# Performance work log

Measured on AMD Instinct MI355X. Metric: run time of the kernel, lower is better.

The kernel has to match this reference:

```python
import jax, jax.numpy as jnp
import numpy as np

T, D, E, F = 8192, 1024, 8, 3584


def setup_inputs() -> dict:
    key = jax.random.key(0)
    ks = jax.random.split(key, 5)
    scale_in = 1.0 / np.sqrt(D)
    scale_ff = 1.0 / np.sqrt(F)
    return {
        "x": jax.random.normal(ks[0], (T, D), dtype=jnp.float32),
        "w1": jax.random.normal(ks[1], (E, F, D), dtype=jnp.float32) * scale_in,
        "w3": jax.random.normal(ks[2], (E, F, D), dtype=jnp.float32) * scale_in,
        "w2": jax.random.normal(ks[3], (E, D, F), dtype=jnp.float32) * scale_ff,
        "router_logits": jax.random.normal(ks[4], (T, E), dtype=jnp.float32),
        "top_k": 2,
    }


def reference(x, w1, w3, w2, router_logits, top_k):
    # Routing: softmax over experts, keep top-k, renormalize (Mixtral, normalize=True)
    probs = jax.nn.softmax(router_logits, axis=-1)            # [T, E]
    top_vals, top_idx = jax.lax.top_k(probs, top_k)           # [T, k]
    top_vals = top_vals / jnp.sum(top_vals, axis=-1, keepdims=True)
    tokens = jnp.arange(x.shape[0])[:, None]
    weights = jnp.zeros_like(probs).at[tokens, top_idx].set(top_vals)  # [T, E]

    gate = jnp.einsum('td,efd->tef', x, w1)                   # [T, E, F]
    up = jnp.einsum('td,efd->tef', x, w3)                     # [T, E, F]
    h = jax.nn.silu(gate) * up                                # [T, E, F]
    out = jnp.einsum('te,tef,edf->td', weights, h, w2)        # [T, D]
    return out
```

## Files before the change

kernel.cpp:

```cpp
#include <hip/hip_runtime.h>
#include <cstdint>

#define T_TOK 8192
#define D_DIM 1024
#define E_EXP 8
#define F_DIM 3584
#define NROW  (2 * T_TOK)

typedef __attribute__((ext_vector_type(8))) __bf16 bf16x8;
typedef __attribute__((ext_vector_type(4))) float f32x4;

__device__ __forceinline__ void gload16(const void* g, void* l) {
    __builtin_amdgcn_global_load_lds(
        (const __attribute__((address_space(1))) void*)(g),
        (__attribute__((address_space(3))) void*)(l),
        16, 0, 0);
}

__device__ __forceinline__ int xcd_swz(int bid, int nwg) {
    const int nx = 8;
    const int q = nwg / nx, r = nwg % nx;
    const int xcd = bid % nx, lid = bid / nx;
    return (xcd < r ? xcd * (q + 1) : r * (q + 1) + (xcd - r) * q) + lid;
}

__global__ void cvt_kernel(const float* __restrict__ in, __bf16* __restrict__ out, long n) {
    long i = ((long)blockIdx.x * blockDim.x + threadIdx.x) * 8;
    if (i >= n) return;
    const float4 f0 = *(const float4*)(in + i);
    const float4 f1 = *(const float4*)(in + i + 4);
    bf16x8 o;
    o[0] = (__bf16)f0.x; o[1] = (__bf16)f0.y; o[2] = (__bf16)f0.z; o[3] = (__bf16)f0.w;
    o[4] = (__bf16)f1.x; o[5] = (__bf16)f1.y; o[6] = (__bf16)f1.z; o[7] = (__bf16)f1.w;
    *(bf16x8*)(out + i) = o;
}

__global__ void route_kernel(const float* __restrict__ rl, int* cnt,
                             int* __restrict__ eidx, float* __restrict__ ewgt) {
    int t = blockIdx.x * blockDim.x + threadIdx.x;
    if (t >= T_TOK) return;
    float l[8];
#pragma unroll
    for (int e = 0; e < 8; ++e) l[e] = rl[t * 8 + e];
    int i0 = 0; float v0 = l[0];
    int i1 = -1; float v1 = -1e30f;
#pragma unroll
    for (int e = 1; e < 8; ++e) {
        if (l[e] > v0) { v1 = v0; i1 = i0; v0 = l[e]; i0 = e; }
        else if (l[e] > v1) { v1 = l[e]; i1 = e; }
    }
    float wsec = 1.f / (1.f + __expf(v0 - v1));
    eidx[2 * t] = i0; eidx[2 * t + 1] = i1;
    ewgt[2 * t] = 1.f - wsec; ewgt[2 * t + 1] = wsec;
    atomicAdd(&cnt[i0], 1); atomicAdd(&cnt[i1], 1);
}

__global__ void scan_kernel(const int* __restrict__ cnt, int* __restrict__ offs) {
    if (threadIdx.x == 0) {
        int a = 0;
        for (int e = 0; e < E_EXP; ++e) { offs[e] = a; a += cnt[e]; }
        offs[E_EXP] = a;
    }
}

__global__ void assign_kernel(const int* __restrict__ eidx, const float* __restrict__ ewgt,
                              const int* __restrict__ offs, int* cnt2,
                              int* __restrict__ tok, int* __restrict__ rowOf) {
    int t = blockIdx.x * blockDim.x + threadIdx.x;
    if (t >= T_TOK) return;
#pragma unroll
    for (int s = 0; s < 2; ++s) {
        int e = eidx[2 * t + s];
        int pos = atomicAdd(&cnt2[e], 1);
        int row = offs[e] + pos;
        tok[row] = t;
        rowOf[2 * t + s] = row;
    }
}

__device__ __forceinline__ int chunk_row(int c) { return ((c >> 7) << 4) | ((c >> 2) & 15); }
__device__ __forceinline__ int chunk_col(int c) {
    return ((c >> 6) & 1) * 32 + (((c & 3) * 8) ^ (((c >> 5) & 1) << 4));
}

template <int NT>
__device__ __forceinline__ void moe_pipeline(
    const __bf16* const (&srcA)[2][2], const __bf16* const (&srcB)[2][2],
    __bf16 (&Ash)[2][2][8192], __bf16 (&Bsh)[2][2][8192],
    int wave, int abase, int wm, int bh, int bsel, f32x4 (&acc)[8][4])
{
    auto stA = [&](int buf, int kt, int h) {
        const int k0 = kt * 64;
        gload16(srcA[h][0] + k0, &Ash[buf][h][(0 * 512 + wave * 64) * 8]);
        gload16(srcA[h][1] + k0, &Ash[buf][h][(1 * 512 + wave * 64) * 8]);
    };
    auto stB = [&](int buf, int kt, int h) {
        const int k0 = kt * 64;
        gload16(srcB[h][0] + k0, &Bsh[buf][h][(0 * 512 + wave * 64) * 8]);
        gload16(srcB[h][1] + k0, &Bsh[buf][h][(1 * 512 + wave * 64) * 8]);
    };

    bf16x8 bfr[4][2];
    bf16x8 a0, a1, a2, a3;

#define LD_A(Ab, q) \
    a0 = *(const bf16x8*)((Ab) + ((2*(q)) * 2 + 0) * 512); \
    a1 = *(const bf16x8*)((Ab) + ((2*(q)) * 2 + 1) * 512); \
    a2 = *(const bf16x8*)((Ab) + ((2*(q)+1) * 2 + 0) * 512); \
    a3 = *(const bf16x8*)((Ab) + ((2*(q)+1) * 2 + 1) * 512);

#define LD_B(Bb) \
    _Pragma("unroll") for (int ni = 0; ni < 4; ++ni) { \
        bfr[ni][0] = *(const bf16x8*)((Bb) + ((bsel * 4 + ni) * 2 + 0) * 512); \
        bfr[ni][1] = *(const bf16x8*)((Bb) + ((bsel * 4 + ni) * 2 + 1) * 512); \
    }

#define MFMA_Q(q) \
    _Pragma("unroll") for (int ni = 0; ni < 4; ++ni) { \
        acc[2*(q)][ni]   = __builtin_amdgcn_mfma_f32_16x16x32_bf16(a0, bfr[ni][0], acc[2*(q)][ni], 0, 0, 0); \
        acc[2*(q)][ni]   = __builtin_amdgcn_mfma_f32_16x16x32_bf16(a1, bfr[ni][1], acc[2*(q)][ni], 0, 0, 0); \
        acc[2*(q)+1][ni] = __builtin_amdgcn_mfma_f32_16x16x32_bf16(a2, bfr[ni][0], acc[2*(q)+1][ni], 0, 0, 0); \
        acc[2*(q)+1][ni] = __builtin_amdgcn_mfma_f32_16x16x32_bf16(a3, bfr[ni][1], acc[2*(q)+1][ni], 0, 0, 0); \
    }

#define PH_OPEN() \
    __builtin_amdgcn_sched_barrier(0); \
    __builtin_amdgcn_s_barrier(); \
    asm volatile("s_waitcnt lgkmcnt(0)" ::: "memory"); \
    __builtin_amdgcn_sched_barrier(0); \
    __builtin_amdgcn_s_setprio(1);

#define PH_CLOSE() \
    __builtin_amdgcn_s_setprio(0); \
    __builtin_amdgcn_sched_barrier(0); \
    __builtin_amdgcn_s_barrier(); \
    __builtin_amdgcn_sched_barrier(0);

#define PH_CLOSE_G(lastf) \
    __builtin_amdgcn_s_setprio(0); \
    __builtin_amdgcn_sched_barrier(0); \
    if (lastf) { asm volatile("s_waitcnt vmcnt(0)" ::: "memory"); } \
    else       { asm volatile("s_waitcnt vmcnt(4)" ::: "memory"); } \
    __builtin_amdgcn_s_barrier(); \
    __builtin_amdgcn_sched_barrier(0);

    stA(0, 0, 0); stA(0, 0, 1); stB(0, 0, 0); stB(0, 0, 1);
    stB(1, 1, 0); stB(1, 1, 1);
    asm volatile("s_waitcnt vmcnt(4)" ::: "memory");
    __builtin_amdgcn_s_barrier();

    const __bf16* AbE = &Ash[0][wm][abase];
    const __bf16* BbE = &Bsh[0][bh][abase];
    const __bf16* AbO = &Ash[1][wm][abase];
    const __bf16* BbO = &Bsh[1][bh][abase];

    for (int it = 0; it < NT / 2; ++it) {
        const int kv = 2 * it + 1;
        const bool last = (it == NT / 2 - 1);
        LD_A(AbE, 0) LD_B(BbE)
        stA(1, kv, 0);
        PH_OPEN() MFMA_Q(0) PH_CLOSE()
        LD_A(AbE, 1)
        stA(1, kv, 1);
        PH_OPEN() MFMA_Q(1) PH_CLOSE()
        LD_A(AbE, 2)
        if (!last) stB(0, kv + 1, 0);
        PH_OPEN() MFMA_Q(2) PH_CLOSE()
        LD_A(AbE, 3)
        if (!last) stB(0, kv + 1, 1);
        PH_OPEN() MFMA_Q(3) PH_CLOSE_G(last)
        LD_A(AbO, 0) LD_B(BbO)
        if (!last) stA(0, kv + 1, 0);
        PH_OPEN() MFMA_Q(0) PH_CLOSE()
        LD_A(AbO, 1)
        if (!last) stA(0, kv + 1, 1);
        PH_OPEN() MFMA_Q(1) PH_CLOSE()
        LD_A(AbO, 2)
        if (!last) stB(1, kv + 2, 0);
        PH_OPEN() MFMA_Q(2) PH_CLOSE()
        LD_A(AbO, 3)
        if (!last) stB(1, kv + 2, 1);
        PH_OPEN() MFMA_Q(3) PH_CLOSE_G(last)
    }
#undef LD_A
#undef LD_B
#undef MFMA_Q
#undef PH_OPEN
#undef PH_CLOSE
#undef PH_CLOSE_G
}

__global__ __launch_bounds__(512, 1)
void gemm1_kernel(const __bf16* __restrict__ xb,
                  const __bf16* __restrict__ w1b,
                  const __bf16* __restrict__ w3b,
                  const int* __restrict__ tok_of_row,
                  const int* __restrict__ offs,
                  __bf16* __restrict__ h) {
    const int NX = F_DIM / 128, NY = T_TOK / 256;
    const int nwg = NX * NY * E_EXP;
    int w = xcd_swz(blockIdx.x + NX * (blockIdx.y + NY * blockIdx.z), nwg);
    const int nt = w % NX; w /= NX;
    const int mt = w % NY; w /= NY;
    const int e = w;
    const int row0 = offs[e];
    const int rows = offs[e + 1] - row0;
    if (mt * 256 >= rows) return;

    __shared__ __align__(16) __bf16 Ash[2][2][8192];
    __shared__ __align__(16) __bf16 Bsh[2][2][8192];

    const int tid = threadIdx.x;
    const int wave = tid >> 6, lane = tid & 63;
    const int wm = wave >> 2, wn = wave & 3;
    const int fr = lane & 15, fg = lane >> 4;

    const __bf16* srcA[2][2];
    const __bf16* srcB[2][2];
#pragma unroll
    for (int half = 0; half < 2; ++half)
#pragma unroll
        for (int j = 0; j < 2; ++j) {
            const int c = tid + j * 512;
            const int r = chunk_row(c), k = chunk_col(c);
            int ra = mt * 256 + half * 128 + r;
            ra = min(ra, rows - 1);
            srcA[half][j] = xb + (long)tok_of_row[row0 + ra] * D_DIM + k;
            const int rb = half * 128 + r;
            const int blk = rb >> 4;
            const int f = nt * 128 + (blk >> 1) * 16 + (rb & 15);
            const __bf16* wsel = (blk & 1) ? w3b : w1b;
            srcB[half][j] = wsel + ((long)e * F_DIM + f) * D_DIM + k;
        }

    const int abase = fr * 32 + ((fg * 8) ^ ((fr & 8) << 1));
    f32x4 acc[8][4] = {};

    moe_pipeline<16>(srcA, srcB, Ash, Bsh, wave, abase, wm, wn >> 1, wn & 1, acc);

#pragma unroll
    for (int mi = 0; mi < 8; ++mi) {
#pragma unroll
        for (int reg = 0; reg < 4; ++reg) {
            const int lm = mt * 256 + wm * 128 + mi * 16 + fg * 4 + reg;
            if (lm < rows) {
                const long hrow = (long)(row0 + lm) * F_DIM;
#pragma unroll
                for (int b = 0; b < 2; ++b) {
                    const float g = acc[mi][2 * b][reg];
                    const float u = acc[mi][2 * b + 1][reg];
                    const float s = g / (1.f + __expf(-g));
                    h[hrow + nt * 128 + (wn * 2 + b) * 16 + fr] = (__bf16)(s * u);
                }
            }
        }
    }
}

__global__ __launch_bounds__(512, 1)
void gemm2_kernel(const __bf16* __restrict__ h,
                  const __bf16* __restrict__ w2b,
                  const int* __restrict__ offs,
                  __bf16* __restrict__ o2p) {
    const int NX = D_DIM / 256, NY = T_TOK / 256, NZ = E_EXP * 4;
    const int nwg = NX * NY * NZ;
    int w = xcd_swz(blockIdx.x + NX * (blockIdx.y + NY * blockIdx.z), nwg);
    const int nt = w % NX; w /= NX;
    const int mt = w % NY; w /= NY;
    const int e = w >> 2, ks = w & 3;
    const int row0 = offs[e];
    const int rows = offs[e + 1] - row0;
    if (mt * 256 >= rows) return;

    __shared__ __align__(16) __bf16 Ash[2][2][8192];
    __shared__ __align__(16) __bf16 Bsh[2][2][8192];

    const int tid = threadIdx.x;
    const int wave = tid >> 6, lane = tid & 63;
    const int wm = wave >> 2, wn = wave & 3;
    const int fr = lane & 15, fg = lane >> 4;
    const int kofs = ks * 14 * 64;

    const __bf16* srcA[2][2];
    const __bf16* srcB[2][2];
#pragma unroll
    for (int half = 0; half < 2; ++half)
#pragma unroll
        for (int j = 0; j < 2; ++j) {
            const int c = tid + j * 512;
            const int r = chunk_row(c), k = chunk_col(c) + kofs;
            int ra = mt * 256 + half * 128 + r;
            ra = min(ra, rows - 1);
            srcA[half][j] = h + (long)(row0 + ra) * F_DIM + k;
            const int rb = half * 128 + r;
            srcB[half][j] = w2b + ((long)e * D_DIM + nt * 256 + rb) * F_DIM + k;
        }

    const int abase = fr * 32 + ((fg * 8) ^ ((fr & 8) << 1));
    f32x4 acc[8][4] = {};

    moe_pipeline<14>(srcA, srcB, Ash, Bsh, wave, abase, wm, wn >> 1, wn & 1, acc);

    __bf16* ps = o2p + (long)ks * NROW * D_DIM;
#pragma unroll
    for (int mi = 0; mi < 8; ++mi) {
#pragma unroll
        for (int reg = 0; reg < 4; ++reg) {
            const int lm = mt * 256 + wm * 128 + mi * 16 + fg * 4 + reg;
            if (lm < rows) {
                const long obase = (long)(row0 + lm) * D_DIM + nt * 256 + wn * 64 + fr;
#pragma unroll
                for (int ni = 0; ni < 4; ++ni)
                    ps[obase + ni * 16] = (__bf16)acc[mi][ni][reg];
            }
        }
    }
}

__global__ void combine_kernel(const __bf16* __restrict__ o2p, const int* __restrict__ rowOf,
                               const float* __restrict__ ewgt, float* __restrict__ out) {
    const int idx = blockIdx.x * blockDim.x + threadIdx.x;
    const int t = idx >> 7;
    const int j = (idx & 127) * 8;
    const long r0 = rowOf[2 * t], r1 = rowOf[2 * t + 1];
    const float w0 = ewgt[2 * t], w1 = ewgt[2 * t + 1];
    float r[8] = {0, 0, 0, 0, 0, 0, 0, 0};
#pragma unroll
    for (int s = 0; s < 4; ++s) {
        const bf16x8 a = *(const bf16x8*)(o2p + ((long)s * NROW + r0) * D_DIM + j);
        const bf16x8 b = *(const bf16x8*)(o2p + ((long)s * NROW + r1) * D_DIM + j);
#pragma unroll
        for (int q = 0; q < 8; ++q) r[q] += w0 * (float)a[q] + w1 * (float)b[q];
    }
    float4* ob = (float4*)(out + (long)t * D_DIM + j);
    ob[0] = make_float4(r[0], r[1], r[2], r[3]);
    ob[1] = make_float4(r[4], r[5], r[6], r[7]);
}

extern "C" void kernel_launch(void* const* d_in, const int* in_sizes, int n_in,
                              void* d_out, int out_size, void* d_ws, size_t ws_size,
                              hipStream_t stream) {
    const float* x  = (const float*)d_in[0];
    const float* w1 = (const float*)d_in[1];
    const float* w3 = (const float*)d_in[2];
    const float* w2 = (const float*)d_in[3];
    const float* rl = (const float*)d_in[4];
    float* out = (float*)d_out;

    char* ws = (char*)d_ws;
    size_t off = 0;
    auto alloc = [&](size_t bytes) {
        void* p = ws + off;
        off += (bytes + 255) & ~(size_t)255;
        return p;
    };
    __bf16* xb   = (__bf16*)alloc((size_t)T_TOK * D_DIM * 2);
    __bf16* w1b  = (__bf16*)alloc((size_t)E_EXP * F_DIM * D_DIM * 2);
    __bf16* w3b  = (__bf16*)alloc((size_t)E_EXP * F_DIM * D_DIM * 2);
    __bf16* w2b  = (__bf16*)alloc((size_t)E_EXP * D_DIM * F_DIM * 2);
    __bf16* h    = (__bf16*)alloc((size_t)NROW * F_DIM * 2);
    int*   tok   = (int*)alloc(NROW * 4);
    int*   rowOf = (int*)alloc(NROW * 4);
    int*   eidx  = (int*)alloc(NROW * 4);
    float* ewgt  = (float*)alloc(NROW * 4);
    int*   cnt1  = (int*)alloc(64);
    int*   cnt2  = (int*)alloc(64);
    int*   offs  = (int*)alloc(64);
    __bf16* o2p  = xb;

    hipMemsetAsync(cnt1, 0, 64, stream);
    hipMemsetAsync(cnt2, 0, 64, stream);

    {
        long n = (long)T_TOK * D_DIM;
        cvt_kernel<<<(int)(n / 8 / 256), 256, 0, stream>>>(x, xb, n);
        n = (long)E_EXP * F_DIM * D_DIM;
        const int blks = (int)(n / 8 / 256);
        cvt_kernel<<<blks, 256, 0, stream>>>(w1, w1b, n);
        cvt_kernel<<<blks, 256, 0, stream>>>(w3, w3b, n);
        cvt_kernel<<<blks, 256, 0, stream>>>(w2, w2b, n);
    }

    route_kernel<<<T_TOK / 256, 256, 0, stream>>>(rl, cnt1, eidx, ewgt);
    scan_kernel<<<1, 64, 0, stream>>>(cnt1, offs);
    assign_kernel<<<T_TOK / 256, 256, 0, stream>>>(eidx, ewgt, offs, cnt2, tok, rowOf);

    dim3 g1(F_DIM / 128, T_TOK / 256, E_EXP);
    gemm1_kernel<<<g1, 512, 0, stream>>>(xb, w1b, w3b, tok, offs, h);

    dim3 g2(D_DIM / 256, T_TOK / 256, E_EXP * 4);
    gemm2_kernel<<<g2, 512, 0, stream>>>(h, w2b, offs, o2p);

    combine_kernel<<<T_TOK * (D_DIM / 8) / 256, 256, 0, stream>>>(o2p, rowOf, ewgt, out);
}
```

Baseline: 709.8 us.

## Gather tokens into padded per-expert rows and retile GEMMs with triple buffering

Adds a gather kernel that casts routed token rows to bf16 in a per-expert buffer padded to multiples of 256. GEMM loads then use contiguous rows with no per-row token indirection or row bounds checks. Both grouped GEMMs move to smaller tiles (64-wide F for gemm1, 128-wide D for gemm2) with a three-stage LDS pipeline, and gemm2's split-K drops from 4 to 2, which halves the partial-sum traffic in combine. The w2 conversion moves to after gemm1 so w2b and o2p can reuse the workspace region. In exchange, padded rows add wasted compute and smaller tiles reduce operand reuse.

```diff
diff --git a/kernel.cpp b/kernel.cpp
--- a/kernel.cpp
+++ b/kernel.cpp
@@ -6,6 +6,7 @@
 #define E_EXP 8
 #define F_DIM 3584
 #define NROW  (2 * T_TOK)
+#define PROWS_PAD 18432
 
 typedef __attribute__((ext_vector_type(8))) __bf16 bf16x8;
 typedef __attribute__((ext_vector_type(4))) float f32x4;
@@ -55,73 +56,48 @@
     atomicAdd(&cnt[i0], 1); atomicAdd(&cnt[i1], 1);
 }
 
-__global__ void scan_kernel(const int* __restrict__ cnt, int* __restrict__ offs) {
+__global__ void scan_kernel(const int* __restrict__ cnt, int* __restrict__ pofs) {
     if (threadIdx.x == 0) {
         int a = 0;
-        for (int e = 0; e < E_EXP; ++e) { offs[e] = a; a += cnt[e]; }
-        offs[E_EXP] = a;
-    }
-}
-
-__global__ void assign_kernel(const int* __restrict__ eidx, const float* __restrict__ ewgt,
-                              const int* __restrict__ offs, int* cnt2,
-                              int* __restrict__ tok, int* __restrict__ rowOf) {
+        for (int e = 0; e < E_EXP; ++e) { pofs[e] = a; a += (cnt[e] + 255) & ~255; }
+        pofs[E_EXP] = a;
+    }
+}
+
+__global__ void assign_kernel(const int* __restrict__ eidx, const int* __restrict__ pofs,
+                              int* cnt2, int* __restrict__ tokOf, int* __restrict__ rowOf) {
     int t = blockIdx.x * blockDim.x + threadIdx.x;
     if (t >= T_TOK) return;
 #pragma unroll
     for (int s = 0; s < 2; ++s) {
         int e = eidx[2 * t + s];
         int pos = atomicAdd(&cnt2[e], 1);
-        int row = offs[e] + pos;
-        tok[row] = t;
-        rowOf[2 * t + s] = row;
-    }
+        int prow = pofs[e] + pos;
+        tokOf[prow] = t;
+        rowOf[2 * t + s] = prow;
+    }
+}
+
+__global__ void gather_kernel(const float* __restrict__ x, const int* __restrict__ tokOf,
+                              __bf16* __restrict__ xg) {
+    const int idx = blockIdx.x * blockDim.x + threadIdx.x;
+    const int pr = idx >> 7;
+    const int j = (idx & 127) * 8;
+    const int tk = tokOf[pr];
+    bf16x8 o = {};
+    if (tk >= 0) {
+        const float4 f0 = *(const float4*)(x + (long)tk * D_DIM + j);
+        const float4 f1 = *(const float4*)(x + (long)tk * D_DIM + j + 4);
+        o[0] = (__bf16)f0.x; o[1] = (__bf16)f0.y; o[2] = (__bf16)f0.z; o[3] = (__bf16)f0.w;
+        o[4] = (__bf16)f1.x; o[5] = (__bf16)f1.y; o[6] = (__bf16)f1.z; o[7] = (__bf16)f1.w;
+    }
+    *(bf16x8*)(xg + (long)pr * D_DIM + j) = o;
 }
 
 __device__ __forceinline__ int chunk_row(int c) { return ((c >> 7) << 4) | ((c >> 2) & 15); }
 __device__ __forceinline__ int chunk_col(int c) {
     return ((c >> 6) & 1) * 32 + (((c & 3) * 8) ^ (((c >> 5) & 1) << 4));
 }
-
-template <int NT>
-__device__ __forceinline__ void moe_pipeline(
-    const __bf16* const (&srcA)[2][2], const __bf16* const (&srcB)[2][2],
-    __bf16 (&Ash)[2][2][8192], __bf16 (&Bsh)[2][2][8192],
-    int wave, int abase, int wm, int bh, int bsel, f32x4 (&acc)[8][4])
-{
-    auto stA = [&](int buf, int kt, int h) {
-        const int k0 = kt * 64;
-        gload16(srcA[h][0] + k0, &Ash[buf][h][(0 * 512 + wave * 64) * 8]);
-        gload16(srcA[h][1] + k0, &Ash[buf][h][(1 * 512 + wave * 64) * 8]);
-    };
-    auto stB = [&](int buf, int kt, int h) {
-        const int k0 = kt * 64;
-        gload16(srcB[h][0] + k0, &Bsh[buf][h][(0 * 512 + wave * 64) * 8]);
-        gload16(srcB[h][1] + k0, &Bsh[buf][h][(1 * 512 + wave * 64) * 8]);
-    };
-
-    bf16x8 bfr[4][2];
-    bf16x8 a0, a1, a2, a3;
-
-#define LD_A(Ab, q) \
-    a0 = *(const bf16x8*)((Ab) + ((2*(q)) * 2 + 0) * 512); \
-    a1 = *(const bf16x8*)((Ab) + ((2*(q)) * 2 + 1) * 512); \
-    a2 = *(const bf16x8*)((Ab) + ((2*(q)+1) * 2 + 0) * 512); \
-    a3 = *(const bf16x8*)((Ab) + ((2*(q)+1) * 2 + 1) * 512);
-
-#define LD_B(Bb) \
-    _Pragma("unroll") for (int ni = 0; ni < 4; ++ni) { \
-        bfr[ni][0] = *(const bf16x8*)((Bb) + ((bsel * 4 + ni) * 2 + 0) * 512); \
-        bfr[ni][1] = *(const bf16x8*)((Bb) + ((bsel * 4 + ni) * 2 + 1) * 512); \
-    }
-
-#define MFMA_Q(q) \
-    _Pragma("unroll") for (int ni = 0; ni < 4; ++ni) { \
-        acc[2*(q)][ni]   = __builtin_amdgcn_mfma_f32_16x16x32_bf16(a0, bfr[ni][0], acc[2*(q)][ni], 0, 0, 0); \
-        acc[2*(q)][ni]   = __builtin_amdgcn_mfma_f32_16x16x32_bf16(a1, bfr[ni][1], acc[2*(q)][ni], 0, 0, 0); \
-        acc[2*(q)+1][ni] = __builtin_amdgcn_mfma_f32_16x16x32_bf16(a2, bfr[ni][0], acc[2*(q)+1][ni], 0, 0, 0); \
-        acc[2*(q)+1][ni] = __builtin_amdgcn_mfma_f32_16x16x32_bf16(a3, bfr[ni][1], acc[2*(q)+1][ni], 0, 0, 0); \
-    }
 
 #define PH_OPEN() \
     __builtin_amdgcn_sched_barrier(0); \
@@ -136,183 +112,203 @@
     __builtin_amdgcn_s_barrier(); \
     __builtin_amdgcn_sched_barrier(0);
 
-#define PH_CLOSE_G(lastf) \
+#define PH_CLOSE_GATE() \
     __builtin_amdgcn_s_setprio(0); \
     __builtin_amdgcn_sched_barrier(0); \
-    if (lastf) { asm volatile("s_waitcnt vmcnt(0)" ::: "memory"); } \
-    else       { asm volatile("s_waitcnt vmcnt(4)" ::: "memory"); } \
+    asm volatile("s_waitcnt vmcnt(8)" ::: "memory"); \
     __builtin_amdgcn_s_barrier(); \
     __builtin_amdgcn_sched_barrier(0);
 
-    stA(0, 0, 0); stA(0, 0, 1); stB(0, 0, 0); stB(0, 0, 1);
-    stB(1, 1, 0); stB(1, 1, 1);
-    asm volatile("s_waitcnt vmcnt(4)" ::: "memory");
+template <int NT>
+__device__ __forceinline__ void moe_pipeline(
+    const __bf16* const (&srcA)[2][2], const __bf16* const (&srcB)[2],
+    __bf16 (&Ash)[3][2][8192], __bf16 (&Bsh)[3][8192],
+    int wave, int abase, int ah, int wqm, int wn, f32x4 (&acc)[4][4])
+{
+    auto stA = [&](int buf, int kt, int h) {
+        const long k0 = (long)kt * 64;
+        gload16(srcA[h][0] + k0, &Ash[buf][h][(0 * 512 + wave * 64) * 8]);
+        gload16(srcA[h][1] + k0, &Ash[buf][h][(1 * 512 + wave * 64) * 8]);
+    };
+    auto stB = [&](int buf, int kt) {
+        const long k0 = (long)kt * 64;
+        gload16(srcB[0] + k0, &Bsh[buf][(0 * 512 + wave * 64) * 8]);
+        gload16(srcB[1] + k0, &Bsh[buf][(1 * 512 + wave * 64) * 8]);
+    };
+
+    stA(0, 0, 0); stA(0, 0, 1); stB(0, 0);
+    stB(1, 1); stA(1, 1, 0); stA(1, 1, 1);
+    stB(2, 2);
+    asm volatile("s_waitcnt vmcnt(8)" ::: "memory");
     __builtin_amdgcn_s_barrier();
 
-    const __bf16* AbE = &Ash[0][wm][abase];
-    const __bf16* BbE = &Bsh[0][bh][abase];
-    const __bf16* AbO = &Ash[1][wm][abase];
-    const __bf16* BbO = &Bsh[1][bh][abase];
-
-    for (int it = 0; it < NT / 2; ++it) {
-        const int kv = 2 * it + 1;
-        const bool last = (it == NT / 2 - 1);
-        LD_A(AbE, 0) LD_B(BbE)
-        stA(1, kv, 0);
-        PH_OPEN() MFMA_Q(0) PH_CLOSE()
-        LD_A(AbE, 1)
-        stA(1, kv, 1);
-        PH_OPEN() MFMA_Q(1) PH_CLOSE()
-        LD_A(AbE, 2)
-        if (!last) stB(0, kv + 1, 0);
-        PH_OPEN() MFMA_Q(2) PH_CLOSE()
-        LD_A(AbE, 3)
-        if (!last) stB(0, kv + 1, 1);
-        PH_OPEN() MFMA_Q(3) PH_CLOSE_G(last)
-        LD_A(AbO, 0) LD_B(BbO)
-        if (!last) stA(0, kv + 1, 0);
-        PH_OPEN() MFMA_Q(0) PH_CLOSE()
-        LD_A(AbO, 1)
-        if (!last) stA(0, kv + 1, 1);
-        PH_OPEN() MFMA_Q(1) PH_CLOSE()
-        LD_A(AbO, 2)
-        if (!last) stB(1, kv + 2, 0);
-        PH_OPEN() MFMA_Q(2) PH_CLOSE()
-        LD_A(AbO, 3)
-        if (!last) stB(1, kv + 2, 1);
-        PH_OPEN() MFMA_Q(3) PH_CLOSE_G(last)
-    }
-#undef LD_A
-#undef LD_B
-#undef MFMA_Q
-#undef PH_OPEN
-#undef PH_CLOSE
-#undef PH_CLOSE_G
+    bf16x8 bfr[4][2], afr[2][2];
+
+#pragma unroll
+    for (int t = 0; t < NT; ++t) {
+        const int b0 = t % 3, b2 = (t + 2) % 3;
+        const int k2 = (t + 2 < NT) ? t + 2 : t + 2 - NT;
+        const int k3 = (t + 3 < NT) ? t + 3 : t + 3 - NT;
+        const __bf16* Ab = &Ash[b0][ah][abase];
+        const __bf16* Bb = &Bsh[b0][abase];
+#pragma unroll
+        for (int ni = 0; ni < 4; ++ni)
+#pragma unroll
+            for (int kk = 0; kk < 2; ++kk)
+                bfr[ni][kk] = *(const bf16x8*)(Bb + ((wn * 4 + ni) * 2 + kk) * 512);
+#pragma unroll
+        for (int mi = 0; mi < 2; ++mi)
+#pragma unroll
+            for (int kk = 0; kk < 2; ++kk)
+                afr[mi][kk] = *(const bf16x8*)(Ab + ((wqm * 4 + mi) * 2 + kk) * 512);
+        PH_OPEN()
+        stA(b2, k2, 0); stA(b2, k2, 1);
+#pragma unroll
+        for (int mi = 0; mi < 2; ++mi)
+#pragma unroll
+            for (int ni = 0; ni < 4; ++ni) {
+                acc[mi][ni] = __builtin_amdgcn_mfma_f32_16x16x32_bf16(afr[mi][0], bfr[ni][0], acc[mi][ni], 0, 0, 0);
+                acc[mi][ni] = __builtin_amdgcn_mfma_f32_16x16x32_bf16(afr[mi][1], bfr[ni][1], acc[mi][ni], 0, 0, 0);
+            }
+        PH_CLOSE()
+#pragma unroll
+        for (int mi = 0; mi < 2; ++mi)
+#pragma unroll
+            for (int kk = 0; kk < 2; ++kk)
+                afr[mi][kk] = *(const bf16x8*)(Ab + ((wqm * 4 + 2 + mi) * 2 + kk) * 512);
+        PH_OPEN()
+        stB(b0, k3);
+#pragma unroll
+        for (int mi = 0; mi < 2; ++mi)
+#pragma unroll
+            for (int ni = 0; ni < 4; ++ni) {
+                acc[2 + mi][ni] = __builtin_amdgcn_mfma_f32_16x16x32_bf16(afr[mi][0], bfr[ni][0], acc[2 + mi][ni], 0, 0, 0);
+                acc[2 + mi][ni] = __builtin_amdgcn_mfma_f32_16x16x32_bf16(afr[mi][1], bfr[ni][1], acc[2 + mi][ni], 0, 0, 0);
+            }
+        PH_CLOSE_GATE()
+    }
+    asm volatile("s_waitcnt vmcnt(0)" ::: "memory");
 }
 
 __global__ __launch_bounds__(512, 1)
-void gemm1_kernel(const __bf16* __restrict__ xb,
+void gemm1_kernel(const __bf16* __restrict__ xg,
                   const __bf16* __restrict__ w1b,
                   const __bf16* __restrict__ w3b,
-                  const int* __restrict__ tok_of_row,
-                  const int* __restrict__ offs,
+                  const int* __restrict__ pofs,
                   __bf16* __restrict__ h) {
-    const int NX = F_DIM / 128, NY = T_TOK / 256;
+    const int NX = F_DIM / 64, NY = T_TOK / 256;
     const int nwg = NX * NY * E_EXP;
     int w = xcd_swz(blockIdx.x + NX * (blockIdx.y + NY * blockIdx.z), nwg);
     const int nt = w % NX; w /= NX;
     const int mt = w % NY; w /= NY;
     const int e = w;
-    const int row0 = offs[e];
-    const int rows = offs[e + 1] - row0;
-    if (mt * 256 >= rows) return;
-
-    __shared__ __align__(16) __bf16 Ash[2][2][8192];
-    __shared__ __align__(16) __bf16 Bsh[2][2][8192];
+    const int row0 = pofs[e];
+    const int prows = pofs[e + 1] - row0;
+    if (mt * 256 >= prows) return;
+
+    __shared__ __align__(16) __bf16 Ash[3][2][8192];
+    __shared__ __align__(16) __bf16 Bsh[3][8192];
 
     const int tid = threadIdx.x;
     const int wave = tid >> 6, lane = tid & 63;
-    const int wm = wave >> 2, wn = wave & 3;
+    const int wm = wave >> 1, wn = wave & 1;
     const int fr = lane & 15, fg = lane >> 4;
 
     const __bf16* srcA[2][2];
-    const __bf16* srcB[2][2];
+    const __bf16* srcB[2];
 #pragma unroll
     for (int half = 0; half < 2; ++half)
 #pragma unroll
         for (int j = 0; j < 2; ++j) {
             const int c = tid + j * 512;
-            const int r = chunk_row(c), k = chunk_col(c);
-            int ra = mt * 256 + half * 128 + r;
-            ra = min(ra, rows - 1);
-            srcA[half][j] = xb + (long)tok_of_row[row0 + ra] * D_DIM + k;
-            const int rb = half * 128 + r;
-            const int blk = rb >> 4;
-            const int f = nt * 128 + (blk >> 1) * 16 + (rb & 15);
-            const __bf16* wsel = (blk & 1) ? w3b : w1b;
-            srcB[half][j] = wsel + ((long)e * F_DIM + f) * D_DIM + k;
+            srcA[half][j] = xg + (long)(row0 + mt * 256 + half * 128 + chunk_row(c)) * D_DIM + chunk_col(c);
         }
+#pragma unroll
+    for (int j = 0; j < 2; ++j) {
+        const int c = tid + j * 512;
+        const int rb = chunk_row(c);
+        const int blk = rb >> 4;
+        const int f = nt * 64 + (blk >> 1) * 16 + (rb & 15);
+        srcB[j] = ((blk & 1) ? w3b : w1b) + ((long)e * F_DIM + f) * D_DIM + chunk_col(c);
+    }
 
     const int abase = fr * 32 + ((fg * 8) ^ ((fr & 8) << 1));
-    f32x4 acc[8][4] = {};
-
-    moe_pipeline<16>(srcA, srcB, Ash, Bsh, wave, abase, wm, wn >> 1, wn & 1, acc);
-
-#pragma unroll
-    for (int mi = 0; mi < 8; ++mi) {
+    f32x4 acc[4][4] = {};
+
+    moe_pipeline<D_DIM / 64>(srcA, srcB, Ash, Bsh, wave, abase, wm >> 1, wm & 1, wn, acc);
+
+#pragma unroll
+    for (int mi = 0; mi < 4; ++mi) {
 #pragma unroll
         for (int reg = 0; reg < 4; ++reg) {
-            const int lm = mt * 256 + wm * 128 + mi * 16 + fg * 4 + reg;
-            if (lm < rows) {
-                const long hrow = (long)(row0 + lm) * F_DIM;
-#pragma unroll
-                for (int b = 0; b < 2; ++b) {
-                    const float g = acc[mi][2 * b][reg];
-                    const float u = acc[mi][2 * b + 1][reg];
-                    const float s = g / (1.f + __expf(-g));
-                    h[hrow + nt * 128 + (wn * 2 + b) * 16 + fr] = (__bf16)(s * u);
-                }
+            const int lm = mt * 256 + wm * 64 + mi * 16 + fg * 4 + reg;
+            const long hrow = (long)(row0 + lm) * F_DIM;
+#pragma unroll
+            for (int b = 0; b < 2; ++b) {
+                const float g = acc[mi][2 * b][reg];
+                const float u = acc[mi][2 * b + 1][reg];
+                const float s = g / (1.f + __expf(-g));
+                h[hrow + nt * 64 + (wn * 2 + b) * 16 + fr] = (__bf16)(s * u);
             }
         }
     }
 }
 
 __global__ __launch_bounds__(512, 1)
-void gemm2_kernel(const __bf16* __restrict__ h,
+void gemm2_kernel(const __bf16* __restrict__ hb,
                   const __bf16* __restrict__ w2b,
-                  const int* __restrict__ offs,
+                  const int* __restrict__ pofs,
                   __bf16* __restrict__ o2p) {
-    const int NX = D_DIM / 256, NY = T_TOK / 256, NZ = E_EXP * 4;
-    const int nwg = NX * NY * NZ;
+    const int NX = D_DIM / 128, NY = T_TOK / 256;
+    const int nwg = NX * NY * E_EXP * 2;
     int w = xcd_swz(blockIdx.x + NX * (blockIdx.y + NY * blockIdx.z), nwg);
     const int nt = w % NX; w /= NX;
     const int mt = w % NY; w /= NY;
-    const int e = w >> 2, ks = w & 3;
-    const int row0 = offs[e];
-    const int rows = offs[e + 1] - row0;
-    if (mt * 256 >= rows) return;
-
-    __shared__ __align__(16) __bf16 Ash[2][2][8192];
-    __shared__ __align__(16) __bf16 Bsh[2][2][8192];
+    const int e = w >> 1, ks = w & 1;
+    const int row0 = pofs[e];
+    const int prows = pofs[e + 1] - row0;
+    if (mt * 256 >= prows) return;
+
+    __shared__ __align__(16) __bf16 Ash[3][2][8192];
+    __shared__ __align__(16) __bf16 Bsh[3][8192];
 
     const int tid = threadIdx.x;
     const int wave = tid >> 6, lane = tid & 63;
-    const int wm = wave >> 2, wn = wave & 3;
+    const int wm = wave >> 1, wn = wave & 1;
     const int fr = lane & 15, fg = lane >> 4;
-    const int kofs = ks * 14 * 64;
+    const int kofs = ks * (F_DIM / 2);
 
     const __bf16* srcA[2][2];
-    const __bf16* srcB[2][2];
+    const __bf16* srcB[2];
 #pragma unroll
     for (int half = 0; half < 2; ++half)
 #pragma unroll
         for (int j = 0; j < 2; ++j) {
             const int c = tid + j * 512;
-            const int r = chunk_row(c), k = chunk_col(c) + kofs;
-            int ra = mt * 256 + half * 128 + r;
-            ra = min(ra, rows - 1);
-            srcA[half][j] = h + (long)(row0 + ra) * F_DIM + k;
-            const int rb = half * 128 + r;
-            srcB[half][j] = w2b + ((long)e * D_DIM + nt * 256 + rb) * F_DIM + k;
+            srcA[half][j] = hb + (long)(row0 + mt * 256 + half * 128 + chunk_row(c)) * F_DIM + kofs + chunk_col(c);
         }
+#pragma unroll
+    for (int j = 0; j < 2; ++j) {
+        const int c = tid + j * 512;
+        const int d = nt * 128 + chunk_row(c);
+        srcB[j] = w2b + ((long)e * D_DIM + d) * F_DIM + kofs + chunk_col(c);
+    }
 
     const int abase = fr * 32 + ((fg * 8) ^ ((fr & 8) << 1));
-    f32x4 acc[8][4] = {};
-
-    moe_pipeline<14>(srcA, srcB, Ash, Bsh, wave, abase, wm, wn >> 1, wn & 1, acc);
-
-    __bf16* ps = o2p + (long)ks * NROW * D_DIM;
-#pragma unroll
-    for (int mi = 0; mi < 8; ++mi) {
+    f32x4 acc[4][4] = {};
+
+    moe_pipeline<F_DIM / 2 / 64>(srcA, srcB, Ash, Bsh, wave, abase, wm >> 1, wm & 1, wn, acc);
+
+    __bf16* ps = o2p + (long)ks * PROWS_PAD * D_DIM;
+#pragma unroll
+    for (int mi = 0; mi < 4; ++mi) {
 #pragma unroll
         for (int reg = 0; reg < 4; ++reg) {
-            const int lm = mt * 256 + wm * 128 + mi * 16 + fg * 4 + reg;
-            if (lm < rows) {
-                const long obase = (long)(row0 + lm) * D_DIM + nt * 256 + wn * 64 + fr;
-#pragma unroll
-                for (int ni = 0; ni < 4; ++ni)
-                    ps[obase + ni * 16] = (__bf16)acc[mi][ni][reg];
-            }
+            const int lm = mt * 256 + wm * 64 + mi * 16 + fg * 4 + reg;
+            const long obase = (long)(row0 + lm) * D_DIM + nt * 128 + wn * 64 + fr;
+#pragma unroll
+            for (int ni = 0; ni < 4; ++ni)
+                ps[obase + ni * 16] = (__bf16)acc[mi][ni][reg];
         }
     }
 }
@@ -326,9 +322,9 @@
     const float w0 = ewgt[2 * t], w1 = ewgt[2 * t + 1];
     float r[8] = {0, 0, 0, 0, 0, 0, 0, 0};
 #pragma unroll
-    for (int s = 0; s < 4; ++s) {
-        const bf16x8 a = *(const bf16x8*)(o2p + ((long)s * NROW + r0) * D_DIM + j);
-        const bf16x8 b = *(const bf16x8*)(o2p + ((long)s * NROW + r1) * D_DIM + j);
+    for (int s = 0; s < 2; ++s) {
+        const bf16x8 a = *(const bf16x8*)(o2p + ((long)s * PROWS_PAD + r0) * D_DIM + j);
+        const bf16x8 b = *(const bf16x8*)(o2p + ((long)s * PROWS_PAD + r1) * D_DIM + j);
 #pragma unroll
         for (int q = 0; q < 8; ++q) r[q] += w0 * (float)a[q] + w1 * (float)b[q];
     }
@@ -354,42 +350,46 @@
         off += (bytes + 255) & ~(size_t)255;
         return p;
     };
-    __bf16* xb   = (__bf16*)alloc((size_t)T_TOK * D_DIM * 2);
+    __bf16* xg   = (__bf16*)alloc((size_t)PROWS_PAD * D_DIM * 2);
     __bf16* w1b  = (__bf16*)alloc((size_t)E_EXP * F_DIM * D_DIM * 2);
     __bf16* w3b  = (__bf16*)alloc((size_t)E_EXP * F_DIM * D_DIM * 2);
-    __bf16* w2b  = (__bf16*)alloc((size_t)E_EXP * D_DIM * F_DIM * 2);
-    __bf16* h    = (__bf16*)alloc((size_t)NROW * F_DIM * 2);
-    int*   tok   = (int*)alloc(NROW * 4);
+    __bf16* hbuf = (__bf16*)alloc((size_t)PROWS_PAD * F_DIM * 2);
+    int*   tokOf = (int*)alloc(PROWS_PAD * 4);
     int*   rowOf = (int*)alloc(NROW * 4);
     int*   eidx  = (int*)alloc(NROW * 4);
     float* ewgt  = (float*)alloc(NROW * 4);
     int*   cnt1  = (int*)alloc(64);
     int*   cnt2  = (int*)alloc(64);
-    int*   offs  = (int*)alloc(64);
-    __bf16* o2p  = xb;
+    int*   pofs  = (int*)alloc(64);
+    __bf16* w2b = (__bf16*)ws;
+    __bf16* o2p = (__bf16*)(ws + (size_t)E_EXP * F_DIM * D_DIM * 2);
 
     hipMemsetAsync(cnt1, 0, 64, stream);
     hipMemsetAsync(cnt2, 0, 64, stream);
+    hipMemsetAsync(tokOf, 0xFF, PROWS_PAD * 4, stream);
+
+    route_kernel<<<T_TOK / 256, 256, 0, stream>>>(rl, cnt1, eidx, ewgt);
+    scan_kernel<<<1, 64, 0, stream>>>(cnt1, pofs);
+    assign_kernel<<<T_TOK / 256, 256, 0, stream>>>(eidx, pofs, cnt2, tokOf, rowOf);
+    gather_kernel<<<PROWS_PAD * 128 / 256, 256, 0, stream>>>(x, tokOf, xg);
 
     {
-        long n = (long)T_TOK * D_DIM;
-        cvt_kernel<<<(int)(n / 8 / 256), 256, 0, stream>>>(x, xb, n);
-        n = (long)E_EXP * F_DIM * D_DIM;
+        const long n = (long)E_EXP * F_DIM * D_DIM;
         const int blks = (int)(n / 8 / 256);
         cvt_kernel<<<blks, 256, 0, stream>>>(w1, w1b, n);
         cvt_kernel<<<blks, 256, 0, stream>>>(w3, w3b, n);
-        cvt_kernel<<<blks, 256, 0, stream>>>(w2, w2b, n);
-    }
-
-    route_kernel<<<T_TOK / 256, 256, 0, stream>>>(rl, cnt1, eidx, ewgt);
-    scan_kernel<<<1, 64, 0, stream>>>(cnt1, offs);
-    assign_kernel<<<T_TOK / 256, 256, 0, stream>>>(eidx, ewgt, offs, cnt2, tok, rowOf);
-
-    dim3 g1(F_DIM / 128, T_TOK / 256, E_EXP);
-    gemm1_kernel<<<g1, 512, 0, stream>>>(xb, w1b, w3b, tok, offs, h);
-
-    dim3 g2(D_DIM / 256, T_TOK / 256, E_EXP * 4);
-    gemm2_kernel<<<g2, 512, 0, stream>>>(h, w2b, offs, o2p);
+    }
+
+    dim3 g1(F_DIM / 64, T_TOK / 256, E_EXP);
+    gemm1_kernel<<<g1, 512, 0, stream>>>(xg, w1b, w3b, pofs, hbuf);
+
+    {
+        const long n = (long)E_EXP * D_DIM * F_DIM;
+        cvt_kernel<<<(int)(n / 8 / 256), 256, 0, stream>>>(w2, w2b, n);
+    }
+
+    dim3 g2(D_DIM / 128, T_TOK / 256, E_EXP * 2);
+    gemm2_kernel<<<g2, 512, 0, stream>>>(hbuf, w2b, pofs, o2p);
 
     combine_kernel<<<T_TOK * (D_DIM / 8) / 256, 256, 0, stream>>>(o2p, rowOf, ewgt, out);
 }
```

After: 821.2 us. 1.16x slower.

## Pre-gather padded per-expert activations and halve gemm2 split-K

Applied to the files above, without the earlier changes.

Routing now runs before conversion. Each expert's row block is padded to a multiple of 256, and a gather kernel writes token rows as bf16 into a contiguous, padded activation buffer. This removes the per-row indirect token lookup and the row-bound checks from gemm1's loads and epilogues, and it folds the x conversion into the gather. gemm2's split-K drops from 4 to 2, which halves the partial-output traffic read back by combine but gives each block a longer K loop and fewer blocks. The workspace is rearranged so w2b and the partials alias earlier buffers, which adds a memset and some wasted work on padded rows.

```diff
diff --git a/kernel.cpp b/kernel.cpp
--- a/kernel.cpp
+++ b/kernel.cpp
@@ -6,6 +6,7 @@
 #define E_EXP 8
 #define F_DIM 3584
 #define NROW  (2 * T_TOK)
+#define PROWS_PAD 18432
 
 typedef __attribute__((ext_vector_type(8))) __bf16 bf16x8;
 typedef __attribute__((ext_vector_type(4))) float f32x4;
@@ -55,27 +56,42 @@
     atomicAdd(&cnt[i0], 1); atomicAdd(&cnt[i1], 1);
 }
 
-__global__ void scan_kernel(const int* __restrict__ cnt, int* __restrict__ offs) {
+__global__ void scan_kernel(const int* __restrict__ cnt, int* __restrict__ pofs) {
     if (threadIdx.x == 0) {
         int a = 0;
-        for (int e = 0; e < E_EXP; ++e) { offs[e] = a; a += cnt[e]; }
-        offs[E_EXP] = a;
-    }
-}
-
-__global__ void assign_kernel(const int* __restrict__ eidx, const float* __restrict__ ewgt,
-                              const int* __restrict__ offs, int* cnt2,
-                              int* __restrict__ tok, int* __restrict__ rowOf) {
+        for (int e = 0; e < E_EXP; ++e) { pofs[e] = a; a += (cnt[e] + 255) & ~255; }
+        pofs[E_EXP] = a;
+    }
+}
+
+__global__ void assign_kernel(const int* __restrict__ eidx, const int* __restrict__ pofs,
+                              int* cnt2, int* __restrict__ tokOf, int* __restrict__ rowOf) {
     int t = blockIdx.x * blockDim.x + threadIdx.x;
     if (t >= T_TOK) return;
 #pragma unroll
     for (int s = 0; s < 2; ++s) {
         int e = eidx[2 * t + s];
         int pos = atomicAdd(&cnt2[e], 1);
-        int row = offs[e] + pos;
-        tok[row] = t;
-        rowOf[2 * t + s] = row;
-    }
+        int prow = pofs[e] + pos;
+        tokOf[prow] = t;
+        rowOf[2 * t + s] = prow;
+    }
+}
+
+__global__ void gather_kernel(const float* __restrict__ x, const int* __restrict__ tokOf,
+                              __bf16* __restrict__ xg) {
+    const int idx = blockIdx.x * blockDim.x + threadIdx.x;
+    const int pr = idx >> 7;
+    const int j = (idx & 127) * 8;
+    const int tk = tokOf[pr];
+    bf16x8 o = {};
+    if (tk >= 0) {
+        const float4 f0 = *(const float4*)(x + (long)tk * D_DIM + j);
+        const float4 f1 = *(const float4*)(x + (long)tk * D_DIM + j + 4);
+        o[0] = (__bf16)f0.x; o[1] = (__bf16)f0.y; o[2] = (__bf16)f0.z; o[3] = (__bf16)f0.w;
+        o[4] = (__bf16)f1.x; o[5] = (__bf16)f1.y; o[6] = (__bf16)f1.z; o[7] = (__bf16)f1.w;
+    }
+    *(bf16x8*)(xg + (long)pr * D_DIM + j) = o;
 }
 
 __device__ __forceinline__ int chunk_row(int c) { return ((c >> 7) << 4) | ((c >> 2) & 15); }
@@ -90,12 +106,12 @@
     int wave, int abase, int wm, int bh, int bsel, f32x4 (&acc)[8][4])
 {
     auto stA = [&](int buf, int kt, int h) {
-        const int k0 = kt * 64;
+        const long k0 = (long)kt * 64;
         gload16(srcA[h][0] + k0, &Ash[buf][h][(0 * 512 + wave * 64) * 8]);
         gload16(srcA[h][1] + k0, &Ash[buf][h][(1 * 512 + wave * 64) * 8]);
     };
     auto stB = [&](int buf, int kt, int h) {
-        const int k0 = kt * 64;
+        const long k0 = (long)kt * 64;
         gload16(srcB[h][0] + k0, &Bsh[buf][h][(0 * 512 + wave * 64) * 8]);
         gload16(srcB[h][1] + k0, &Bsh[buf][h][(1 * 512 + wave * 64) * 8]);
     };
@@ -191,11 +207,10 @@
 }
 
 __global__ __launch_bounds__(512, 1)
-void gemm1_kernel(const __bf16* __restrict__ xb,
+void gemm1_kernel(const __bf16* __restrict__ xg,
                   const __bf16* __restrict__ w1b,
                   const __bf16* __restrict__ w3b,
-                  const int* __restrict__ tok_of_row,
-                  const int* __restrict__ offs,
+                  const int* __restrict__ pofs,
                   __bf16* __restrict__ h) {
     const int NX = F_DIM / 128, NY = T_TOK / 256;
     const int nwg = NX * NY * E_EXP;
@@ -203,9 +218,9 @@
     const int nt = w % NX; w /= NX;
     const int mt = w % NY; w /= NY;
     const int e = w;
-    const int row0 = offs[e];
-    const int rows = offs[e + 1] - row0;
-    if (mt * 256 >= rows) return;
+    const int row0 = pofs[e];
+    const int prows = pofs[e + 1] - row0;
+    if (mt * 256 >= prows) return;
 
     __shared__ __align__(16) __bf16 Ash[2][2][8192];
     __shared__ __align__(16) __bf16 Bsh[2][2][8192];
@@ -222,15 +237,11 @@
 #pragma unroll
         for (int j = 0; j < 2; ++j) {
             const int c = tid + j * 512;
-            const int r = chunk_row(c), k = chunk_col(c);
-            int ra = mt * 256 + half * 128 + r;
-            ra = min(ra, rows - 1);
-            srcA[half][j] = xb + (long)tok_of_row[row0 + ra] * D_DIM + k;
-            const int rb = half * 128 + r;
+            srcA[half][j] = xg + (long)(row0 + mt * 256 + half * 128 + chunk_row(c)) * D_DIM + chunk_col(c);
+            const int rb = half * 128 + chunk_row(c);
             const int blk = rb >> 4;
             const int f = nt * 128 + (blk >> 1) * 16 + (rb & 15);
-            const __bf16* wsel = (blk & 1) ? w3b : w1b;
-            srcB[half][j] = wsel + ((long)e * F_DIM + f) * D_DIM + k;
+            srcB[half][j] = ((blk & 1) ? w3b : w1b) + ((long)e * F_DIM + f) * D_DIM + chunk_col(c);
         }
 
     const int abase = fr * 32 + ((fg * 8) ^ ((fr & 8) << 1));
@@ -243,34 +254,32 @@
 #pragma unroll
         for (int reg = 0; reg < 4; ++reg) {
             const int lm = mt * 256 + wm * 128 + mi * 16 + fg * 4 + reg;
-            if (lm < rows) {
-                const long hrow = (long)(row0 + lm) * F_DIM;
-#pragma unroll
-                for (int b = 0; b < 2; ++b) {
-                    const float g = acc[mi][2 * b][reg];
-                    const float u = acc[mi][2 * b + 1][reg];
-                    const float s = g / (1.f + __expf(-g));
-                    h[hrow + nt * 128 + (wn * 2 + b) * 16 + fr] = (__bf16)(s * u);
-                }
+            const long hrow = (long)(row0 + lm) * F_DIM;
+#pragma unroll
+            for (int b = 0; b < 2; ++b) {
+                const float g = acc[mi][2 * b][reg];
+                const float u = acc[mi][2 * b + 1][reg];
+                const float s = g / (1.f + __expf(-g));
+                h[hrow + nt * 128 + (wn * 2 + b) * 16 + fr] = (__bf16)(s * u);
             }
         }
     }
 }
 
 __global__ __launch_bounds__(512, 1)
-void gemm2_kernel(const __bf16* __restrict__ h,
+void gemm2_kernel(const __bf16* __restrict__ hb,
                   const __bf16* __restrict__ w2b,
-                  const int* __restrict__ offs,
+                  const int* __restrict__ pofs,
                   __bf16* __restrict__ o2p) {
-    const int NX = D_DIM / 256, NY = T_TOK / 256, NZ = E_EXP * 4;
-    const int nwg = NX * NY * NZ;
+    const int NX = D_DIM / 256, NY = T_TOK / 256;
+    const int nwg = NX * NY * E_EXP * 2;
     int w = xcd_swz(blockIdx.x + NX * (blockIdx.y + NY * blockIdx.z), nwg);
     const int nt = w % NX; w /= NX;
     const int mt = w % NY; w /= NY;
-    const int e = w >> 2, ks = w & 3;
-    const int row0 = offs[e];
-    const int rows = offs[e + 1] - row0;
-    if (mt * 256 >= rows) return;
+    const int e = w >> 1, ks = w & 1;
+    const int row0 = pofs[e];
+    const int prows = pofs[e + 1] - row0;
+    if (mt * 256 >= prows) return;
 
     __shared__ __align__(16) __bf16 Ash[2][2][8192];
     __shared__ __align__(16) __bf16 Bsh[2][2][8192];
@@ -279,7 +288,7 @@
     const int wave = tid >> 6, lane = tid & 63;
     const int wm = wave >> 2, wn = wave & 3;
     const int fr = lane & 15, fg = lane >> 4;
-    const int kofs = ks * 14 * 64;
+    const int kofs = ks * (F_DIM / 2);
 
     const __bf16* srcA[2][2];
     const __bf16* srcB[2][2];
@@ -288,31 +297,26 @@
 #pragma unroll
         for (int j = 0; j < 2; ++j) {
             const int c = tid + j * 512;
-            const int r = chunk_row(c), k = chunk_col(c) + kofs;
-            int ra = mt * 256 + half * 128 + r;
-            ra = min(ra, rows - 1);
-            srcA[half][j] = h + (long)(row0 + ra) * F_DIM + k;
-            const int rb = half * 128 + r;
-            srcB[half][j] = w2b + ((long)e * D_DIM + nt * 256 + rb) * F_DIM + k;
+            srcA[half][j] = hb + (long)(row0 + mt * 256 + half * 128 + chunk_row(c)) * F_DIM + kofs + chunk_col(c);
+            const int rb = half * 128 + chunk_row(c);
+            srcB[half][j] = w2b + ((long)e * D_DIM + nt * 256 + rb) * F_DIM + kofs + chunk_col(c);
         }
 
     const int abase = fr * 32 + ((fg * 8) ^ ((fr & 8) << 1));
     f32x4 acc[8][4] = {};
 
-    moe_pipeline<14>(srcA, srcB, Ash, Bsh, wave, abase, wm, wn >> 1, wn & 1, acc);
-
-    __bf16* ps = o2p + (long)ks * NROW * D_DIM;
+    moe_pipeline<28>(srcA, srcB, Ash, Bsh, wave, abase, wm, wn >> 1, wn & 1, acc);
+
+    __bf16* ps = o2p + (long)ks * PROWS_PAD * D_DIM;
 #pragma unroll
     for (int mi = 0; mi < 8; ++mi) {
 #pragma unroll
         for (int reg = 0; reg < 4; ++reg) {
             const int lm = mt * 256 + wm * 128 + mi * 16 + fg * 4 + reg;
-            if (lm < rows) {
-                const long obase = (long)(row0 + lm) * D_DIM + nt * 256 + wn * 64 + fr;
-#pragma unroll
-                for (int ni = 0; ni < 4; ++ni)
-                    ps[obase + ni * 16] = (__bf16)acc[mi][ni][reg];
-            }
+            const long obase = (long)(row0 + lm) * D_DIM + nt * 256 + wn * 64 + fr;
+#pragma unroll
+            for (int ni = 0; ni < 4; ++ni)
+                ps[obase + ni * 16] = (__bf16)acc[mi][ni][reg];
         }
     }
 }
@@ -326,9 +330,9 @@
     const float w0 = ewgt[2 * t], w1 = ewgt[2 * t + 1];
     float r[8] = {0, 0, 0, 0, 0, 0, 0, 0};
 #pragma unroll
-    for (int s = 0; s < 4; ++s) {
-        const bf16x8 a = *(const bf16x8*)(o2p + ((long)s * NROW + r0) * D_DIM + j);
-        const bf16x8 b = *(const bf16x8*)(o2p + ((long)s * NROW + r1) * D_DIM + j);
+    for (int s = 0; s < 2; ++s) {
+        const bf16x8 a = *(const bf16x8*)(o2p + ((long)s * PROWS_PAD + r0) * D_DIM + j);
+        const bf16x8 b = *(const bf16x8*)(o2p + ((long)s * PROWS_PAD + r1) * D_DIM + j);
 #pragma unroll
         for (int q = 0; q < 8; ++q) r[q] += w0 * (float)a[q] + w1 * (float)b[q];
     }
@@ -354,42 +358,46 @@
         off += (bytes + 255) & ~(size_t)255;
         return p;
     };
-    __bf16* xb   = (__bf16*)alloc((size_t)T_TOK * D_DIM * 2);
+    __bf16* xg   = (__bf16*)alloc((size_t)PROWS_PAD * D_DIM * 2);
     __bf16* w1b  = (__bf16*)alloc((size_t)E_EXP * F_DIM * D_DIM * 2);
     __bf16* w3b  = (__bf16*)alloc((size_t)E_EXP * F_DIM * D_DIM * 2);
-    __bf16* w2b  = (__bf16*)alloc((size_t)E_EXP * D_DIM * F_DIM * 2);
-    __bf16* h    = (__bf16*)alloc((size_t)NROW * F_DIM * 2);
-    int*   tok   = (int*)alloc(NROW * 4);
+    __bf16* hbuf = (__bf16*)alloc((size_t)PROWS_PAD * F_DIM * 2);
+    int*   tokOf = (int*)alloc(PROWS_PAD * 4);
     int*   rowOf = (int*)alloc(NROW * 4);
     int*   eidx  = (int*)alloc(NROW * 4);
     float* ewgt  = (float*)alloc(NROW * 4);
     int*   cnt1  = (int*)alloc(64);
     int*   cnt2  = (int*)alloc(64);
-    int*   offs  = (int*)alloc(64);
-    __bf16* o2p  = xb;
+    int*   pofs  = (int*)alloc(64);
+    __bf16* w2b = (__bf16*)ws;
+    __bf16* o2p = (__bf16*)(ws + (size_t)E_EXP * D_DIM * F_DIM * 2);
 
     hipMemsetAsync(cnt1, 0, 64, stream);
     hipMemsetAsync(cnt2, 0, 64, stream);
+    hipMemsetAsync(tokOf, 0xFF, PROWS_PAD * 4, stream);
+
+    route_kernel<<<T_TOK / 256, 256, 0, stream>>>(rl, cnt1, eidx, ewgt);
+    scan_kernel<<<1, 64, 0, stream>>>(cnt1, pofs);
+    assign_kernel<<<T_TOK / 256, 256, 0, stream>>>(eidx, pofs, cnt2, tokOf, rowOf);
+    gather_kernel<<<PROWS_PAD * 128 / 256, 256, 0, stream>>>(x, tokOf, xg);
 
     {
-        long n = (long)T_TOK * D_DIM;
-        cvt_kernel<<<(int)(n / 8 / 256), 256, 0, stream>>>(x, xb, n);
-        n = (long)E_EXP * F_DIM * D_DIM;
+        const long n = (long)E_EXP * F_DIM * D_DIM;
         const int blks = (int)(n / 8 / 256);
         cvt_kernel<<<blks, 256, 0, stream>>>(w1, w1b, n);
         cvt_kernel<<<blks, 256, 0, stream>>>(w3, w3b, n);
-        cvt_kernel<<<blks, 256, 0, stream>>>(w2, w2b, n);
-    }
-
-    route_kernel<<<T_TOK / 256, 256, 0, stream>>>(rl, cnt1, eidx, ewgt);
-    scan_kernel<<<1, 64, 0, stream>>>(cnt1, offs);
-    assign_kernel<<<T_TOK / 256, 256, 0, stream>>>(eidx, ewgt, offs, cnt2, tok, rowOf);
+    }
 
     dim3 g1(F_DIM / 128, T_TOK / 256, E_EXP);
-    gemm1_kernel<<<g1, 512, 0, stream>>>(xb, w1b, w3b, tok, offs, h);
-
-    dim3 g2(D_DIM / 256, T_TOK / 256, E_EXP * 4);
-    gemm2_kernel<<<g2, 512, 0, stream>>>(h, w2b, offs, o2p);
+    gemm1_kernel<<<g1, 512, 0, stream>>>(xg, w1b, w3b, pofs, hbuf);
+
+    {
+        const long n = (long)E_EXP * D_DIM * F_DIM;
+        cvt_kernel<<<(int)(n / 8 / 256), 256, 0, stream>>>(w2, w2b, n);
+    }
+
+    dim3 g2(D_DIM / 256, T_TOK / 256, E_EXP * 2);
+    gemm2_kernel<<<g2, 512, 0, stream>>>(hbuf, w2b, pofs, o2p);
 
     combine_kernel<<<T_TOK * (D_DIM / 8) / 256, 256, 0, stream>>>(o2p, rowOf, ewgt, out);
 }
```

Result: no change. 701.5 us (-1.2%).
